# Kernel tuning notes

Hardware: AMD Instinct MI355X
Metric: run time of the kernel (lower is better)

Reference implementation:

```python
import jax, jax.numpy as jnp
import numpy as np

N_NODES = 100000
N_MESH_E = 400000
N_WORLD_E = 200000
D = 128


def setup_inputs() -> dict:
    key = jax.random.key(0)
    ks = jax.random.split(key, 12)
    s = lambda fan_in: 1.0 / np.sqrt(fan_in)
    return {
        "x": jax.random.normal(ks[0], (N_NODES, D), jnp.float32),
        "edge_attr": jax.random.normal(ks[1], (N_MESH_E, D), jnp.float32),
        "edge_index": jax.random.randint(ks[2], (2, N_MESH_E), 0, N_NODES, jnp.int64),
        "world_edge_attr": jax.random.normal(ks[3], (N_WORLD_E, D), jnp.float32),
        "world_edge_index": jax.random.randint(ks[4], (2, N_WORLD_E), 0, N_NODES, jnp.int64),
        "W1": jax.random.normal(ks[5], (3 * D, D), jnp.float32) * s(3 * D),
        "b1": jnp.zeros((D,), jnp.float32),
        "W2": jax.random.normal(ks[6], (D, D), jnp.float32) * s(D),
        "b2": jnp.zeros((D,), jnp.float32),
        "W3": jax.random.normal(ks[7], (D, D), jnp.float32) * s(D),
        "b3": jnp.zeros((D,), jnp.float32),
        "ln_gamma": jnp.ones((D,), jnp.float32),
        "ln_beta": jnp.zeros((D,), jnp.float32),
    }


def _layer_norm(h, gamma, beta, eps=1e-5):
    mu = jnp.mean(h, axis=-1, keepdims=True)
    var = jnp.var(h, axis=-1, keepdims=True)
    return (h - mu) * jax.lax.rsqrt(var + eps) * gamma + beta


def reference(x, edge_attr, edge_index, world_edge_attr, world_edge_index,
              W1, b1, W2, b2, W3, b3, ln_gamma, ln_beta):
    num_nodes = x.shape[0]
    # scatter-sum aggregation from mesh edges to receiver nodes
    mesh_recv = edge_index[1]
    mesh_agg = jax.ops.segment_sum(edge_attr, mesh_recv, num_segments=num_nodes)
    # scatter-sum aggregation from world edges
    world_recv = world_edge_index[1]
    world_agg = jax.ops.segment_sum(world_edge_attr, world_recv, num_segments=num_nodes)
    # concat + MLP (2 hidden ReLU layers) + LayerNorm (MeshGraphNets custom_func)
    collected = jnp.concatenate([x, mesh_agg, world_agg], axis=-1)  # [N, 3D]
    h = jax.nn.relu(collected @ W1 + b1)
    h = jax.nn.relu(h @ W2 + b2)
    h = h @ W3 + b3
    out = _layer_norm(h, ln_gamma, ln_beta)
    return out
```

## Files before the change

### kernel.cpp

```cpp
#include <hip/hip_runtime.h>
#include <hip/hip_bf16.h>
#include <stdint.h>

#define NN  100000
#define NME 400000
#define NWE 200000

typedef __bf16 bf16;
typedef __bf16 bf16x8 __attribute__((ext_vector_type(8)));
typedef float  f32x4  __attribute__((ext_vector_type(4)));

static __device__ __forceinline__ bf16 f2bf(float f) {
    union { unsigned int i; float f; } v; v.f = f;
    unsigned int r = (v.i + 0x7fffu + ((v.i >> 16) & 1u)) >> 16;
    union { unsigned short s; bf16 b; } u; u.s = (unsigned short)r;
    return u.b;
}

__global__ void prep_weights(const float* __restrict__ W1, const float* __restrict__ W2,
                             const float* __restrict__ W3, bf16* __restrict__ W1t,
                             bf16* __restrict__ W2t, bf16* __restrict__ W3t) {
    int tid = blockIdx.x * 256 + threadIdx.x;
    if (tid < 49152) {
        int k = tid >> 7, n = tid & 127;
        W1t[n * 384 + k] = f2bf(W1[tid]);
    } else if (tid < 65536) {
        int t2 = tid - 49152;
        int k = t2 >> 7, n = t2 & 127;
        W2t[n * 128 + k] = f2bf(W2[t2]);
    } else if (tid < 81920) {
        int t2 = tid - 65536;
        int k = t2 >> 7, n = t2 & 127;
        W3t[n * 128 + k] = f2bf(W3[t2]);
    }
}

__global__ __launch_bounds__(256) void count_edges(const int* __restrict__ mrecv,
                                                   const int* __restrict__ wrecv,
                                                   int* __restrict__ mdeg,
                                                   int* __restrict__ wdeg) {
    int t = blockIdx.x * 256 + threadIdx.x;
    if (t < NME) {
        atomicAdd(mdeg + mrecv[t], 1);
    } else {
        int t2 = t - NME;
        if (t2 < NWE) atomicAdd(wdeg + wrecv[t2], 1);
    }
}

__global__ __launch_bounds__(256) void scan_part(const int* __restrict__ mdeg,
                                                 const int* __restrict__ wdeg,
                                                 int* __restrict__ bsum) {
    const int nblk = 25;
    int seg = blockIdx.x / nblk;
    int blk = blockIdx.x % nblk;
    const int* deg = (seg == 0) ? mdeg : wdeg;
    const int t = threadIdx.x;
    const int base = blk * 4096;
    int sum = 0;
#pragma unroll
    for (int i = 0; i < 4; ++i) {
        int idx = base + (i * 256 + t) * 4;
        if (idx < NN) {
            int4 v = *(const int4*)(deg + idx);
            sum += v.x + v.y + v.z + v.w;
        }
    }
#pragma unroll
    for (int m = 1; m < 64; m <<= 1) sum += __shfl_xor(sum, m, 64);
    __shared__ int ssum[4];
    if ((t & 63) == 0) ssum[t >> 6] = sum;
    __syncthreads();
    if (t == 0) bsum[blockIdx.x] = ssum[0] + ssum[1] + ssum[2] + ssum[3];
}

__global__ __launch_bounds__(256) void scan_write(int* __restrict__ mdeg, int* __restrict__ wdeg,
                                                  int* __restrict__ mcur, int* __restrict__ wcur,
                                                  const int* __restrict__ bsum) {
    __shared__ int sprefix;
    __shared__ int sscan[256];
    const int nblk = 25;
    int seg = blockIdx.x / nblk;
    int blk = blockIdx.x % nblk;
    int* deg = (seg == 0) ? mdeg : wdeg;
    int* cur = (seg == 0) ? mcur : wcur;
    const int t = threadIdx.x;
    if (t == 0) {
        int s = 0;
        const int* bs = bsum + seg * nblk;
        for (int i = 0; i < blk; ++i) s += bs[i];
        sprefix = s;
    }
    const int base = blk * 4096 + t * 16;
    int v[16];
#pragma unroll
    for (int i = 0; i < 16; i += 4) {
        int idx = base + i;
        if (idx < NN) {
            int4 q = *(const int4*)(deg + idx);
            v[i] = q.x; v[i + 1] = q.y; v[i + 2] = q.z; v[i + 3] = q.w;
        } else {
            v[i] = v[i + 1] = v[i + 2] = v[i + 3] = 0;
        }
    }
    int lsum = 0;
#pragma unroll
    for (int i = 0; i < 16; ++i) lsum += v[i];
    sscan[t] = lsum;
    __syncthreads();
    for (int d = 1; d < 256; d <<= 1) {
        int vv = (t >= d) ? sscan[t - d] : 0;
        __syncthreads();
        sscan[t] += vv;
        __syncthreads();
    }
    int run = sprefix + sscan[t] - lsum;
#pragma unroll
    for (int i = 0; i < 16; i += 4) {
        int idx = base + i;
        if (idx < NN) {
            int4 o;
            o.x = run; run += v[i];
            o.y = run; run += v[i + 1];
            o.z = run; run += v[i + 2];
            o.w = run; run += v[i + 3];
            *(int4*)(deg + idx) = o;
            *(int4*)(cur + idx) = o;
        }
    }
}

__global__ __launch_bounds__(256) void fill_lists(const int* __restrict__ mrecv,
                                                  const int* __restrict__ wrecv,
                                                  int* __restrict__ mcur, int* __restrict__ wcur,
                                                  int* __restrict__ mlist, int* __restrict__ wlist) {
    int t = blockIdx.x * 256 + threadIdx.x;
    if (t < NME) {
        int r = mrecv[t];
        int p = atomicAdd(mcur + r, 1);
        mlist[p] = t;
    } else {
        int t2 = t - NME;
        if (t2 < NWE) {
            int r = wrecv[t2];
            int p = atomicAdd(wcur + r, 1);
            wlist[p] = t2;
        }
    }
}

__global__ __launch_bounds__(256) void gather_sum(const float* __restrict__ attr,
                                                  const int* __restrict__ off,
                                                  const int* __restrict__ list,
                                                  bf16* __restrict__ agg, int nE) {
    int t = blockIdx.x * 256 + threadIdx.x;
    int node = t >> 4;
    int g = t & 15;
    if (node >= NN) return;
    int j0 = off[node];
    int j1 = (node == NN - 1) ? nE : off[node + 1];
    f32x4 lo = (f32x4)0.0f, hi = (f32x4)0.0f;
    for (int j = j0; j < j1; ++j) {
        int e = list[j];
        const float* src = attr + (size_t)e * 128 + g * 8;
        f32x4 a = *(const f32x4*)(src);
        f32x4 b = *(const f32x4*)(src + 4);
        lo += a;
        hi += b;
    }
    bf16x8 o;
#pragma unroll
    for (int i = 0; i < 4; ++i) {
        o[i]     = f2bf(lo[i]);
        o[4 + i] = f2bf(hi[i]);
    }
    *(bf16x8*)(agg + (size_t)node * 128 + g * 8) = o;
}

static __device__ __forceinline__ const int4* wsrc(const bf16* __restrict__ W1t,
                                                   const bf16* __restrict__ W2t,
                                                   const bf16* __restrict__ W3t,
                                                   int slice, int n, int q) {
    const bf16* W; int ld, kb;
    if (slice < 12)      { W = W1t; ld = 384; kb = slice * 32; }
    else if (slice < 16) { W = W2t; ld = 128; kb = (slice - 12) * 32; }
    else                 { W = W3t; ld = 128; kb = (slice - 16) * 32; }
    return (const int4*)(W + n * ld + kb + q * 8);
}

__global__ __launch_bounds__(256) void node_mlp(
    const float* __restrict__ x, const bf16* __restrict__ magg,
    const bf16* __restrict__ wagg, const bf16* __restrict__ W1t,
    const bf16* __restrict__ W2t, const bf16* __restrict__ W3t,
    const float* __restrict__ b1, const float* __restrict__ b2,
    const float* __restrict__ b3, const float* __restrict__ gam,
    const float* __restrict__ bet, float* __restrict__ out) {
    __shared__ bf16 sh_w[2][4096];
    __shared__ bf16 sh_h[4][32 * 136];
    const int tid  = threadIdx.x;
    const int wave = tid >> 6;
    const int lane = tid & 63;
    const int quad = lane >> 4;
    const int l16  = lane & 15;
    const int node_base = blockIdx.x * 128 + wave * 32;
    bf16* shw = sh_h[wave];

    const int s0 = tid, s1 = tid + 256;
    const int n0 = ((s0 >> 6) << 4) | (s0 & 15), q0 = (s0 >> 4) & 3;
    const int n1 = ((s1 >> 6) << 4) | (s1 & 15), q1 = (s1 >> 4) & 3;
    int4 st0, st1;

    st0 = *wsrc(W1t, W2t, W3t, 0, n0, q0);
    st1 = *wsrc(W1t, W2t, W3t, 0, n1, q1);
    *(int4*)(&sh_w[0][s0 * 8]) = st0;
    *(int4*)(&sh_w[0][s1 * 8]) = st1;
    __syncthreads();

    int arow[2];
    arow[0] = node_base + l16;
    arow[1] = node_base + 16 + l16;
    if (arow[0] >= NN) arow[0] = NN - 1;
    if (arow[1] >= NN) arow[1] = NN - 1;

    f32x4 acc[2][8];
#pragma unroll
    for (int rg = 0; rg < 2; ++rg)
#pragma unroll
        for (int t = 0; t < 8; ++t) acc[rg][t] = (f32x4)0.0f;

#pragma unroll
    for (int ks = 0; ks < 12; ++ks) {
        st0 = *wsrc(W1t, W2t, W3t, ks + 1, n0, q0);
        st1 = *wsrc(W1t, W2t, W3t, ks + 1, n1, q1);
        int kg = ks * 32 + quad * 8;
        bf16x8 af[2];
#pragma unroll
        for (int rg = 0; rg < 2; ++rg) {
            if (ks < 4) {
                const float* src = x + (size_t)arow[rg] * 128 + kg;
                f32x4 lo = *(const f32x4*)(src);
                f32x4 hi = *(const f32x4*)(src + 4);
#pragma unroll
                for (int i = 0; i < 4; ++i) {
                    af[rg][i]     = f2bf(lo[i]);
                    af[rg][4 + i] = f2bf(hi[i]);
                }
            } else if (ks < 8) {
                af[rg] = *(const bf16x8*)(magg + (size_t)arow[rg] * 128 + (kg - 128));
            } else {
                af[rg] = *(const bf16x8*)(wagg + (size_t)arow[rg] * 128 + (kg - 256));
            }
        }
        const bf16* wb = sh_w[ks & 1];
#pragma unroll
        for (int t = 0; t < 8; ++t) {
            bf16x8 bfrag = *(const bf16x8*)(wb + t * 512 + lane * 8);
            acc[0][t] = __builtin_amdgcn_mfma_f32_16x16x32_bf16(af[0], bfrag, acc[0][t], 0, 0, 0);
            acc[1][t] = __builtin_amdgcn_mfma_f32_16x16x32_bf16(af[1], bfrag, acc[1][t], 0, 0, 0);
        }
        __syncthreads();
        *(int4*)(&sh_w[(ks + 1) & 1][s0 * 8]) = st0;
        *(int4*)(&sh_w[(ks + 1) & 1][s1 * 8]) = st1;
        __syncthreads();
    }
#pragma unroll
    for (int t = 0; t < 8; ++t) {
        float bv = b1[t * 16 + l16];
#pragma unroll
        for (int rg = 0; rg < 2; ++rg)
#pragma unroll
            for (int r = 0; r < 4; ++r) {
                float h = acc[rg][t][r] + bv;
                h = h > 0.0f ? h : 0.0f;
                shw[(rg * 16 + quad * 4 + r) * 136 + t * 16 + l16] = f2bf(h);
            }
    }

#pragma unroll
    for (int rg = 0; rg < 2; ++rg)
#pragma unroll
        for (int t = 0; t < 8; ++t) acc[rg][t] = (f32x4)0.0f;
#pragma unroll
    for (int ks = 0; ks < 4; ++ks) {
        st0 = *wsrc(W1t, W2t, W3t, 13 + ks, n0, q0);
        st1 = *wsrc(W1t, W2t, W3t, 13 + ks, n1, q1);
        bf16x8 a2[2];
        a2[0] = *(const bf16x8*)(shw + l16 * 136 + ks * 32 + quad * 8);
        a2[1] = *(const bf16x8*)(shw + (16 + l16) * 136 + ks * 32 + quad * 8);
        const bf16* wb = sh_w[ks & 1];
#pragma unroll
        for (int t = 0; t < 8; ++t) {
            bf16x8 bfrag = *(const bf16x8*)(wb + t * 512 + lane * 8);
            acc[0][t] = __builtin_amdgcn_mfma_f32_16x16x32_bf16(a2[0], bfrag, acc[0][t], 0, 0, 0);
            acc[1][t] = __builtin_amdgcn_mfma_f32_16x16x32_bf16(a2[1], bfrag, acc[1][t], 0, 0, 0);
        }
        __syncthreads();
        *(int4*)(&sh_w[(13 + ks) & 1][s0 * 8]) = st0;
        *(int4*)(&sh_w[(13 + ks) & 1][s1 * 8]) = st1;
        __syncthreads();
    }
#pragma unroll
    for (int t = 0; t < 8; ++t) {
        float bv = b2[t * 16 + l16];
#pragma unroll
        for (int rg = 0; rg < 2; ++rg)
#pragma unroll
            for (int r = 0; r < 4; ++r) {
                float h = acc[rg][t][r] + bv;
                h = h > 0.0f ? h : 0.0f;
                shw[(rg * 16 + quad * 4 + r) * 136 + t * 16 + l16] = f2bf(h);
            }
    }

#pragma unroll
    for (int rg = 0; rg < 2; ++rg)
#pragma unroll
        for (int t = 0; t < 8; ++t) acc[rg][t] = (f32x4)0.0f;
#pragma unroll
    for (int ks = 0; ks < 4; ++ks) {
        if (ks < 3) {
            st0 = *wsrc(W1t, W2t, W3t, 17 + ks, n0, q0);
            st1 = *wsrc(W1t, W2t, W3t, 17 + ks, n1, q1);
        }
        bf16x8 a2[2];
        a2[0] = *(const bf16x8*)(shw + l16 * 136 + ks * 32 + quad * 8);
        a2[1] = *(const bf16x8*)(shw + (16 + l16) * 136 + ks * 32 + quad * 8);
        const bf16* wb = sh_w[ks & 1];
#pragma unroll
        for (int t = 0; t < 8; ++t) {
            bf16x8 bfrag = *(const bf16x8*)(wb + t * 512 + lane * 8);
            acc[0][t] = __builtin_amdgcn_mfma_f32_16x16x32_bf16(a2[0], bfrag, acc[0][t], 0, 0, 0);
            acc[1][t] = __builtin_amdgcn_mfma_f32_16x16x32_bf16(a2[1], bfrag, acc[1][t], 0, 0, 0);
        }
        if (ks < 3) {
            __syncthreads();
            *(int4*)(&sh_w[(17 + ks) & 1][s0 * 8]) = st0;
            *(int4*)(&sh_w[(17 + ks) & 1][s1 * 8]) = st1;
            __syncthreads();
        }
    }
#pragma unroll
    for (int t = 0; t < 8; ++t) {
        float bv = b3[t * 16 + l16];
#pragma unroll
        for (int rg = 0; rg < 2; ++rg)
#pragma unroll
            for (int r = 0; r < 4; ++r) acc[rg][t][r] += bv;
    }

    float gv[8], bv2[8];
#pragma unroll
    for (int t = 0; t < 8; ++t) {
        gv[t]  = gam[t * 16 + l16];
        bv2[t] = bet[t * 16 + l16];
    }
#pragma unroll
    for (int rg = 0; rg < 2; ++rg) {
        float mean[4], rstd[4];
#pragma unroll
        for (int r = 0; r < 4; ++r) {
            float s = 0.0f, s2 = 0.0f;
#pragma unroll
            for (int t = 0; t < 8; ++t) {
                float v = acc[rg][t][r];
                s += v;
                s2 += v * v;
            }
#pragma unroll
            for (int m = 1; m < 16; m <<= 1) {
                s  += __shfl_xor(s, m, 64);
                s2 += __shfl_xor(s2, m, 64);
            }
            float mu = s * (1.0f / 128.0f);
            float var = s2 * (1.0f / 128.0f) - mu * mu;
            mean[r] = mu;
            rstd[r] = rsqrtf(var + 1e-5f);
        }
#pragma unroll
        for (int r = 0; r < 4; ++r) {
            int row = node_base + rg * 16 + quad * 4 + r;
            if (row < NN) {
#pragma unroll
                for (int t = 0; t < 8; ++t) {
                    float o = (acc[rg][t][r] - mean[r]) * rstd[r] * gv[t] + bv2[t];
                    out[(size_t)row * 128 + t * 16 + l16] = o;
                }
            }
        }
    }
}

extern "C" void kernel_launch(void* const* d_in, const int* in_sizes, int n_in,
                              void* d_out, int out_size, void* d_ws, size_t ws_size,
                              hipStream_t stream) {
    const float* x   = (const float*)d_in[0];
    const float* ea  = (const float*)d_in[1];
    const int*   ei  = (const int*)d_in[2];
    const float* wea = (const float*)d_in[3];
    const int*   wei = (const int*)d_in[4];
    const float* W1  = (const float*)d_in[5];
    const float* b1  = (const float*)d_in[6];
    const float* W2  = (const float*)d_in[7];
    const float* b2  = (const float*)d_in[8];
    const float* W3  = (const float*)d_in[9];
    const float* b3  = (const float*)d_in[10];
    const float* gam = (const float*)d_in[11];
    const float* bet = (const float*)d_in[12];

    char* ws = (char*)d_ws;
    bf16* magg = (bf16*)(ws);
    bf16* wagg = (bf16*)(ws + 25600000);
    bf16* W1t  = (bf16*)(ws + 51200000);
    bf16* W2t  = (bf16*)(ws + 51298304);
    bf16* W3t  = (bf16*)(ws + 51331072);
    int*  mdeg = (int*)(ws + 51363840);
    int*  wdeg = (int*)(ws + 51763840);
    int*  mcur = (int*)(ws + 52163840);
    int*  wcur = (int*)(ws + 52563840);
    int*  mlist = (int*)(ws + 52963840);
    int*  wlist = (int*)(ws + 54563840);
    int*  bsum  = (int*)(ws + 55363840);

    hipMemsetAsync(ws + 51363840, 0, 800000, stream);

    prep_weights<<<320, 256, 0, stream>>>(W1, W2, W3, W1t, W2t, W3t);

    count_edges<<<(NME + NWE + 255) / 256, 256, 0, stream>>>(ei + NME, wei + NWE, mdeg, wdeg);
    scan_part<<<50, 256, 0, stream>>>(mdeg, wdeg, bsum);
    scan_write<<<50, 256, 0, stream>>>(mdeg, wdeg, mcur, wcur, bsum);
    fill_lists<<<(NME + NWE + 255) / 256, 256, 0, stream>>>(ei + NME, wei + NWE,
                                                            mcur, wcur, mlist, wlist);

    gather_sum<<<(NN * 16 + 255) / 256, 256, 0, stream>>>(ea, mdeg, mlist, magg, NME);
    gather_sum<<<(NN * 16 + 255) / 256, 256, 0, stream>>>(wea, wdeg, wlist, wagg, NWE);

    node_mlp<<<(NN + 127) / 128, 256, 0, stream>>>(x, magg, wagg, W1t, W2t, W3t,
                                                   b1, b2, b3, gam, bet, (float*)d_out);
}
```

Before: 539.0 us.

## Merge gathers and x bf16 conversion into one launch; prefetch A fragments in MLP

Result: no change. 531.0 us (-1.5%).

```diff
diff --git a/kernel.cpp b/kernel.cpp
--- a/kernel.cpp
+++ b/kernel.cpp
@@ -149,11 +149,40 @@
     }
 }
 
-__global__ __launch_bounds__(256) void gather_sum(const float* __restrict__ attr,
-                                                  const int* __restrict__ off,
-                                                  const int* __restrict__ list,
-                                                  bf16* __restrict__ agg, int nE) {
-    int t = blockIdx.x * 256 + threadIdx.x;
+__global__ __launch_bounds__(256) void gather_sum2(const float* __restrict__ mattr,
+                                                   const int* __restrict__ moff,
+                                                   const int* __restrict__ mlist,
+                                                   bf16* __restrict__ magg,
+                                                   const float* __restrict__ wattr,
+                                                   const int* __restrict__ woff,
+                                                   const int* __restrict__ wlist,
+                                                   bf16* __restrict__ wagg,
+                                                   const float* __restrict__ x,
+                                                   bf16* __restrict__ xb) {
+    const int nblk = (NN * 16) / 256;
+    if (blockIdx.x >= 2 * nblk) {
+        int blk = blockIdx.x - 2 * nblk;
+        int base = blk * 2048 + threadIdx.x * 8;
+        f32x4 lo = *(const f32x4*)(x + base);
+        f32x4 hi = *(const f32x4*)(x + base + 4);
+        bf16x8 o;
+#pragma unroll
+        for (int i = 0; i < 4; ++i) {
+            o[i]     = f2bf(lo[i]);
+            o[4 + i] = f2bf(hi[i]);
+        }
+        *(bf16x8*)(xb + base) = o;
+        return;
+    }
+    int seg = (blockIdx.x >= nblk);
+    int blk = blockIdx.x - seg * nblk;
+    const float* attr = seg ? wattr : mattr;
+    const int*   off  = seg ? woff  : moff;
+    const int*   list = seg ? wlist : mlist;
+    bf16*        agg  = seg ? wagg  : magg;
+    const int    nE   = seg ? NWE   : NME;
+
+    int t = blk * 256 + threadIdx.x;
     int node = t >> 4;
     int g = t & 15;
     if (node >= NN) return;
@@ -188,8 +217,16 @@
     return (const int4*)(W + n * ld + kb + q * 8);
 }
 
+static __device__ __forceinline__ const bf16x8* asrc(const bf16* __restrict__ xb,
+                                                     const bf16* __restrict__ magg,
+                                                     const bf16* __restrict__ wagg,
+                                                     int ks, int arow, int colq) {
+    const bf16* B = (ks < 4) ? xb : (ks < 8 ? magg : wagg);
+    return (const bf16x8*)(B + (size_t)arow * 128 + (ks & 3) * 32 + colq);
+}
+
 __global__ __launch_bounds__(256) void node_mlp(
-    const float* __restrict__ x, const bf16* __restrict__ magg,
+    const bf16* __restrict__ xb, const bf16* __restrict__ magg,
     const bf16* __restrict__ wagg, const bf16* __restrict__ W1t,
     const bf16* __restrict__ W2t, const bf16* __restrict__ W3t,
     const float* __restrict__ b1, const float* __restrict__ b2,
@@ -222,41 +259,33 @@
     if (arow[0] >= NN) arow[0] = NN - 1;
     if (arow[1] >= NN) arow[1] = NN - 1;
 
+    const int colq = quad * 8;
+
     f32x4 acc[2][8];
 #pragma unroll
     for (int rg = 0; rg < 2; ++rg)
 #pragma unroll
         for (int t = 0; t < 8; ++t) acc[rg][t] = (f32x4)0.0f;
+
+    bf16x8 preA[2];
+    preA[0] = *asrc(xb, magg, wagg, 0, arow[0], colq);
+    preA[1] = *asrc(xb, magg, wagg, 0, arow[1], colq);
 
 #pragma unroll
     for (int ks = 0; ks < 12; ++ks) {
         st0 = *wsrc(W1t, W2t, W3t, ks + 1, n0, q0);
         st1 = *wsrc(W1t, W2t, W3t, ks + 1, n1, q1);
-        int kg = ks * 32 + quad * 8;
-        bf16x8 af[2];
-#pragma unroll
-        for (int rg = 0; rg < 2; ++rg) {
-            if (ks < 4) {
-                const float* src = x + (size_t)arow[rg] * 128 + kg;
-                f32x4 lo = *(const f32x4*)(src);
-                f32x4 hi = *(const f32x4*)(src + 4);
-#pragma unroll
-                for (int i = 0; i < 4; ++i) {
-                    af[rg][i]     = f2bf(lo[i]);
-                    af[rg][4 + i] = f2bf(hi[i]);
-                }
-            } else if (ks < 8) {
-                af[rg] = *(const bf16x8*)(magg + (size_t)arow[rg] * 128 + (kg - 128));
-            } else {
-                af[rg] = *(const bf16x8*)(wagg + (size_t)arow[rg] * 128 + (kg - 256));
-            }
+        bf16x8 af0 = preA[0], af1 = preA[1];
+        if (ks < 11) {
+            preA[0] = *asrc(xb, magg, wagg, ks + 1, arow[0], colq);
+            preA[1] = *asrc(xb, magg, wagg, ks + 1, arow[1], colq);
         }
         const bf16* wb = sh_w[ks & 1];
 #pragma unroll
         for (int t = 0; t < 8; ++t) {
             bf16x8 bfrag = *(const bf16x8*)(wb + t * 512 + lane * 8);
-            acc[0][t] = __builtin_amdgcn_mfma_f32_16x16x32_bf16(af[0], bfrag, acc[0][t], 0, 0, 0);
-            acc[1][t] = __builtin_amdgcn_mfma_f32_16x16x32_bf16(af[1], bfrag, acc[1][t], 0, 0, 0);
+            acc[0][t] = __builtin_amdgcn_mfma_f32_16x16x32_bf16(af0, bfrag, acc[0][t], 0, 0, 0);
+            acc[1][t] = __builtin_amdgcn_mfma_f32_16x16x32_bf16(af1, bfrag, acc[1][t], 0, 0, 0);
         }
         __syncthreads();
         *(int4*)(&sh_w[(ks + 1) & 1][s0 * 8]) = st0;
@@ -285,8 +314,8 @@
         st0 = *wsrc(W1t, W2t, W3t, 13 + ks, n0, q0);
         st1 = *wsrc(W1t, W2t, W3t, 13 + ks, n1, q1);
         bf16x8 a2[2];
-        a2[0] = *(const bf16x8*)(shw + l16 * 136 + ks * 32 + quad * 8);
-        a2[1] = *(const bf16x8*)(shw + (16 + l16) * 136 + ks * 32 + quad * 8);
+        a2[0] = *(const bf16x8*)(shw + l16 * 136 + ks * 32 + colq);
+        a2[1] = *(const bf16x8*)(shw + (16 + l16) * 136 + ks * 32 + colq);
         const bf16* wb = sh_w[ks & 1];
 #pragma unroll
         for (int t = 0; t < 8; ++t) {
@@ -323,8 +352,8 @@
             st1 = *wsrc(W1t, W2t, W3t, 17 + ks, n1, q1);
         }
         bf16x8 a2[2];
-        a2[0] = *(const bf16x8*)(shw + l16 * 136 + ks * 32 + quad * 8);
-        a2[1] = *(const bf16x8*)(shw + (16 + l16) * 136 + ks * 32 + quad * 8);
+        a2[0] = *(const bf16x8*)(shw + l16 * 136 + ks * 32 + colq);
+        a2[1] = *(const bf16x8*)(shw + (16 + l16) * 136 + ks * 32 + colq);
         const bf16* wb = sh_w[ks & 1];
 #pragma unroll
         for (int t = 0; t < 8; ++t) {
@@ -420,6 +449,7 @@
     int*  mlist = (int*)(ws + 52963840);
     int*  wlist = (int*)(ws + 54563840);
     int*  bsum  = (int*)(ws + 55363840);
+    bf16* xb    = (bf16*)(ws + 55364096);
 
     hipMemsetAsync(ws + 51363840, 0, 800000, stream);
 
@@ -431,9 +461,10 @@
     fill_lists<<<(NME + NWE + 255) / 256, 256, 0, stream>>>(ei + NME, wei + NWE,
                                                             mcur, wcur, mlist, wlist);
 
-    gather_sum<<<(NN * 16 + 255) / 256, 256, 0, stream>>>(ea, mdeg, mlist, magg, NME);
-    gather_sum<<<(NN * 16 + 255) / 256, 256, 0, stream>>>(wea, wdeg, wlist, wagg, NWE);
-
-    node_mlp<<<(NN + 127) / 128, 256, 0, stream>>>(x, magg, wagg, W1t, W2t, W3t,
+    gather_sum2<<<3 * ((NN * 16) / 256), 256, 0, stream>>>(ea, mdeg, mlist, magg,
+                                                           wea, wdeg, wlist, wagg,
+                                                           x, xb);
+
+    node_mlp<<<(NN + 127) / 128, 256, 0, stream>>>(xb, magg, wagg, W1t, W2t, W3t,
                                                    b1, b2, b3, gam, bet, (float*)d_out);
 }
```
